# Kernel tuning notes

Hardware: AMD Instinct MI355X
Metric: run time of the kernel (lower is better)

## Reference

```python
import jax, jax.numpy as jnp
import numpy as np

DIM = 2048
N_HEADS = 32
N_KV_HEADS = 8
HEAD_DIM = DIM // N_HEADS  # 64
N_REP = N_HEADS // N_KV_HEADS  # 4
ROPE_BASE = 10000.0


def _rope_cos_sin(seq_len, head_dim, dtype):
    inv_freq = 1.0 / (ROPE_BASE ** (jnp.arange(0, head_dim, 2, dtype=jnp.float32) / head_dim))
    freqs = jnp.arange(seq_len, dtype=jnp.float32)[:, None] * inv_freq[None, :]  # [S, hd/2]
    return jnp.cos(freqs).astype(dtype), jnp.sin(freqs).astype(dtype)


def _apply_rope(x, cos, sin):
    # x: [B, S, H, hd]; cos/sin: [S, hd/2]
    x1, x2 = jnp.split(x, 2, axis=-1)
    c = cos[None, :, None, :]
    s = sin[None, :, None, :]
    return jnp.concatenate([x1 * c - x2 * s, x1 * s + x2 * c], axis=-1)


def setup_inputs() -> dict:
    key = jax.random.key(0)
    ks = jax.random.split(key, 5)
    B, S = 2, 2048
    x = jax.random.normal(ks[0], (B, S, DIM), dtype=jnp.float32)
    scale = 1.0 / np.sqrt(DIM)
    wq = jax.random.normal(ks[1], (DIM, DIM), dtype=jnp.float32) * scale
    wk = jax.random.normal(ks[2], (N_KV_HEADS * HEAD_DIM, DIM), dtype=jnp.float32) * scale
    wv = jax.random.normal(ks[3], (N_KV_HEADS * HEAD_DIM, DIM), dtype=jnp.float32) * scale
    wo = jax.random.normal(ks[4], (DIM, DIM), dtype=jnp.float32) * scale
    return {"x": x, "wq": wq, "wk": wk, "wv": wv, "wo": wo}


def reference(x, wq, wk, wv, wo):
    B, S, D = x.shape
    # projections (nn.Linear: y = x @ W.T)
    xq = (x @ wq.T).reshape(B, S, N_HEADS, HEAD_DIM)
    xk = (x @ wk.T).reshape(B, S, N_KV_HEADS, HEAD_DIM)
    xv = (x @ wv.T).reshape(B, S, N_KV_HEADS, HEAD_DIM)

    cos, sin = _rope_cos_sin(S, HEAD_DIM, x.dtype)
    xq = _apply_rope(xq, cos, sin)
    xk = _apply_rope(xk, cos, sin)

    # GQA: repeat kv heads
    keys = jnp.repeat(xk, N_REP, axis=2)    # [B, S, H, hd]
    values = jnp.repeat(xv, N_REP, axis=2)

    scores = jnp.einsum('bqhd,bkhd->bhqk', xq, keys) / np.sqrt(HEAD_DIM)
    causal = jnp.tril(jnp.ones((S, S), dtype=bool))
    scores = jnp.where(causal[None, None, :, :], scores, jnp.finfo(scores.dtype).min)
    probs = jax.nn.softmax(scores, axis=-1)
    out = jnp.einsum('bhqk,bkhd->bqhd', probs, values).reshape(B, S, D)
    return out @ wo.T  # dropout in eval mode == identity
```

## Files before the change

kernel.cpp:

```cpp
#include <hip/hip_runtime.h>

typedef __attribute__((ext_vector_type(8))) short bf16x8;
typedef __attribute__((ext_vector_type(4))) float f32x4;
typedef __attribute__((ext_vector_type(4))) unsigned short u16x4;

#define GPTR(p) (const __attribute__((address_space(1))) void*)(p)
#define LPTR(p) (__attribute__((address_space(3))) void*)(p)

static __device__ __forceinline__ unsigned short f2bf(float f) {
  union { float f; unsigned int u; } x; x.f = f;
  unsigned int u = x.u;
  unsigned int r = (u + 0x7fffu + ((u >> 16) & 1u)) >> 16;
  return (unsigned short)r;
}
static __device__ __forceinline__ float bf2f(unsigned short h) {
  union { unsigned int u; float f; } x; x.u = ((unsigned int)h) << 16;
  return x.f;
}
static __device__ __forceinline__ f32x4 f32x4_zero() {
  f32x4 z = {0.f, 0.f, 0.f, 0.f}; return z;
}
static __device__ __forceinline__ unsigned int cvt_pk_bf16(float lo, float hi) {
  unsigned int r;
  asm("v_cvt_pk_bf16_f32 %0, %1, %2" : "=v"(r) : "v"(lo), "v"(hi));
  return r;
}

__global__ void rope_table_kernel(float* __restrict__ costab, float* __restrict__ sintab) {
  int i = blockIdx.x * blockDim.x + threadIdx.x;
  int s = i >> 5, d = i & 31;
  float invf = exp2f(-(float)d * (13.287712379549449f / 32.0f));
  float a = (float)s * invf;
  costab[i] = cosf(a);
  sintab[i] = sinf(a);
}

__global__ void f32_to_bf16(const float* __restrict__ src, unsigned short* __restrict__ dst, int n4) {
  int stride = gridDim.x * blockDim.x;
  for (int i = blockIdx.x * blockDim.x + threadIdx.x; i < n4; i += stride) {
    float4 v = ((const float4*)src)[i];
    u16x4 o;
    o.x = f2bf(v.x); o.y = f2bf(v.y); o.z = f2bf(v.z); o.w = f2bf(v.w);
    *(u16x4*)(dst + (size_t)i * 4) = o;
  }
}

template<int OUT_BF16>
__global__ __launch_bounds__(256) void gemm_bt(const unsigned short* __restrict__ A,
                                               const unsigned short* __restrict__ B,
                                               void* __restrict__ Cv, int N, int K) {
  __shared__ __align__(16) unsigned short lsA[128 * 32];
  __shared__ __align__(16) unsigned short lsB[128 * 32];
  const int tid = threadIdx.x;
  const int wave = tid >> 6, lane = tid & 63;
  const int fq = lane >> 4, fr = lane & 15;
  const int wr = wave >> 1, wc = wave & 1;
  const int m0 = blockIdx.y * 128, n0 = blockIdx.x * 128;

  const unsigned short* ga0 = A + (size_t)(m0 + (tid >> 2)) * K + ((tid & 3) << 3);
  const unsigned short* ga1 = ga0 + (size_t)64 * K;
  const unsigned short* gb0 = B + (size_t)(n0 + (tid >> 2)) * K + ((tid & 3) << 3);
  const unsigned short* gb1 = gb0 + (size_t)64 * K;
  unsigned short* lA0 = lsA + wave * 512;
  unsigned short* lA1 = lsA + 2048 + wave * 512;
  unsigned short* lB0 = lsB + wave * 512;
  unsigned short* lB1 = lsB + 2048 + wave * 512;

  f32x4 acc[4][4];
#pragma unroll
  for (int i = 0; i < 4; ++i)
#pragma unroll
    for (int j = 0; j < 4; ++j) acc[i][j] = f32x4_zero();

  for (int k0 = 0; k0 < K; k0 += 32) {
    __syncthreads();
    __builtin_amdgcn_global_load_lds(GPTR(ga0 + k0), LPTR(lA0), 16, 0, 0);
    __builtin_amdgcn_global_load_lds(GPTR(ga1 + k0), LPTR(lA1), 16, 0, 0);
    __builtin_amdgcn_global_load_lds(GPTR(gb0 + k0), LPTR(lB0), 16, 0, 0);
    __builtin_amdgcn_global_load_lds(GPTR(gb1 + k0), LPTR(lB1), 16, 0, 0);
    __syncthreads();
    bf16x8 af[4], bfr[4];
#pragma unroll
    for (int f = 0; f < 4; ++f) {
      af[f]  = *(const bf16x8*)(lsA + (wr * 64 + f * 16 + fr) * 32 + fq * 8);
      bfr[f] = *(const bf16x8*)(lsB + (wc * 64 + f * 16 + fr) * 32 + fq * 8);
    }
#pragma unroll
    for (int i = 0; i < 4; ++i)
#pragma unroll
      for (int j = 0; j < 4; ++j)
        acc[i][j] = __builtin_amdgcn_mfma_f32_16x16x32_bf16(af[i], bfr[j], acc[i][j], 0, 0, 0);
  }

#pragma unroll
  for (int i = 0; i < 4; ++i) {
    const int row = m0 + wr * 64 + i * 16 + fq * 4;
#pragma unroll
    for (int j = 0; j < 4; ++j) {
      const int col = n0 + wc * 64 + j * 16 + fr;
#pragma unroll
      for (int v = 0; v < 4; ++v) {
        if (OUT_BF16) ((unsigned short*)Cv)[(size_t)(row + v) * N + col] = f2bf(acc[i][j][v]);
        else          ((float*)Cv)[(size_t)(row + v) * N + col] = acc[i][j][v];
      }
    }
  }
}

__global__ void rope_kernel(unsigned short* __restrict__ qkv,
                            const float* __restrict__ costab,
                            const float* __restrict__ sintab) {
  int idx = blockIdx.x * blockDim.x + threadIdx.x;
  if (idx >= 4096 * 1280) return;
  int row = idx / 1280;
  int p = idx - row * 1280;
  int s = row & 2047;
  int col, d; bool isq;
  if (p < 1024) { isq = true;  d = p & 31; col = (p >> 5) * 64 + d; }
  else { isq = false; int pk = p - 1024; d = pk & 31; col = 2048 + (pk >> 5) * 64 + d; }
  float c = costab[s * 32 + d], sn = sintab[s * 32 + d];
  unsigned short* base = qkv + (size_t)row * 3072;
  float x1 = bf2f(base[col]), x2 = bf2f(base[col + 32]);
  float o1 = x1 * c - x2 * sn;
  float o2 = x1 * sn + x2 * c;
  if (isq) { o1 *= 0.18033688011112042f; o2 *= 0.18033688011112042f; }
  base[col] = f2bf(o1);
  base[col + 32] = f2bf(o2);
}

#define KBLK 64
__global__ __launch_bounds__(256) void flash_attn(const unsigned short* __restrict__ qkv,
                                                  unsigned short* __restrict__ out) {
  __shared__ __align__(16) unsigned short K_lds[64 * 64];
  __shared__ __align__(16) unsigned short Vt_lds[64 * 64];
  __shared__ __align__(16) unsigned int  P_lds[4][32 * 36];

  const int tid = threadIdx.x;
  const int wave = tid >> 6, lane = tid & 63;
  const int fq = lane >> 4, fr = lane & 15;
  const int b = blockIdx.z, h = blockIdx.y;
  const int qt = gridDim.x - 1 - blockIdx.x;
  const int kvh = h >> 2;
  const int q0 = qt * 128;
  const int wq0 = q0 + wave * 32;

  bf16x8 qreg[2][2];
#pragma unroll
  for (int qf = 0; qf < 2; ++qf)
#pragma unroll
    for (int kk = 0; kk < 2; ++kk)
      qreg[qf][kk] = *(const bf16x8*)(qkv + (size_t)(b * 2048 + wq0 + qf * 16 + fr) * 3072
                                      + h * 64 + kk * 32 + fq * 8);

  f32x4 o_acc[4][2];
  float m_run[2], l_run[2];
#pragma unroll
  for (int dc = 0; dc < 4; ++dc) { o_acc[dc][0] = f32x4_zero(); o_acc[dc][1] = f32x4_zero(); }
  m_run[0] = m_run[1] = -1e30f;
  l_run[0] = l_run[1] = 0.f;

  const char* kgbase = (const char*)qkv + (size_t)(b * 2048) * 6144 + 4096 + kvh * 128;
  const unsigned short* vgbase = qkv + (size_t)(b * 2048) * 3072 + 2560 + kvh * 64;
  const int nsteps = (q0 + 128) >> 6;

  for (int st = 0; st < nsteps; ++st) {
    const int k0 = st << 6;
    __syncthreads();
#pragma unroll
    for (int r = 0; r < 2; ++r) {
      const int row = (tid >> 3) + r * 32;
      const int cb = (tid & 7) << 4;
      __builtin_amdgcn_global_load_lds(GPTR(kgbase + (size_t)(k0 + row) * 6144 + (cb ^ ((row & 7) << 4))),
                                       LPTR((char*)K_lds + r * 4096 + wave * 1024), 16, 0, 0);
    }
#pragma unroll
    for (int r = 0; r < 2; ++r) {
      const int k = (tid >> 3) + r * 32;
      const int c0 = (tid & 7) << 3;
      bf16x8 vv = *(const bf16x8*)(vgbase + (size_t)(k0 + k) * 3072 + c0);
#pragma unroll
      for (int j = 0; j < 8; ++j) {
        const int d = c0 + j;
        Vt_lds[d * 64 + (k & 7) + ((((k >> 3) ^ (d >> 3)) & 7) << 3)] = (unsigned short)vv[j];
      }
    }
    __syncthreads();

    if (k0 <= wq0 + 31) {
      f32x4 s[2][4];
#pragma unroll
      for (int qf = 0; qf < 2; ++qf)
#pragma unroll
        for (int kf = 0; kf < 4; ++kf) s[qf][kf] = f32x4_zero();
#pragma unroll
      for (int kf = 0; kf < 4; ++kf) {
        const int krow = kf * 16 + fr;
        const char* kb = (const char*)K_lds + krow * 128;
        const int swz = (krow & 7) << 4;
        bf16x8 kf0 = *(const bf16x8*)(kb + ((fq * 16) ^ swz));
        bf16x8 kf1 = *(const bf16x8*)(kb + ((64 + fq * 16) ^ swz));
#pragma unroll
        for (int qf = 0; qf < 2; ++qf) {
          s[qf][kf] = __builtin_amdgcn_mfma_f32_16x16x32_bf16(kf0, qreg[qf][0], s[qf][kf], 0, 0, 0);
          s[qf][kf] = __builtin_amdgcn_mfma_f32_16x16x32_bf16(kf1, qreg[qf][1], s[qf][kf], 0, 0, 0);
        }
      }
      if (k0 + 63 > wq0) {
#pragma unroll
        for (int qf = 0; qf < 2; ++qf) {
          const int q = wq0 + qf * 16 + fr;
#pragma unroll
          for (int kf = 0; kf < 4; ++kf)
#pragma unroll
            for (int v = 0; v < 4; ++v) {
              const int key = k0 + kf * 16 + fq * 4 + v;
              if (key > q) s[qf][kf][v] = -1e30f;
            }
        }
      }
#pragma unroll
      for (int qf = 0; qf < 2; ++qf) {
        float t = s[qf][0][0];
#pragma unroll
        for (int kf = 0; kf < 4; ++kf)
#pragma unroll
          for (int v = 0; v < 4; ++v) t = fmaxf(t, s[qf][kf][v]);
        t = fmaxf(t, __shfl_xor(t, 16));
        t = fmaxf(t, __shfl_xor(t, 32));
        const float mo = m_run[qf];
        const float mn = fmaxf(mo, t);
        const float sc = __builtin_amdgcn_exp2f(mo - mn);
        m_run[qf] = mn;
        float ps = 0.f;
#pragma unroll
        for (int kf = 0; kf < 4; ++kf)
#pragma unroll
          for (int v = 0; v < 4; ++v) {
            const float p = __builtin_amdgcn_exp2f(s[qf][kf][v] - mn);
            s[qf][kf][v] = p;
            ps += p;
          }
        ps += __shfl_xor(ps, 16);
        ps += __shfl_xor(ps, 32);
        l_run[qf] = l_run[qf] * sc + ps;
#pragma unroll
        for (int dc = 0; dc < 4; ++dc) o_acc[dc][qf] *= sc;
        unsigned int* pbase = &P_lds[wave][(qf * 16 + fr) * 36];
#pragma unroll
        for (int kf = 0; kf < 4; ++kf) {
          uint2 w;
          w.x = cvt_pk_bf16(s[qf][kf][0], s[qf][kf][1]);
          w.y = cvt_pk_bf16(s[qf][kf][2], s[qf][kf][3]);
          *(uint2*)(pbase + kf * 8 + fq * 2) = w;
        }
      }
#pragma unroll
      for (int kk = 0; kk < 2; ++kk) {
        bf16x8 pa0 = *(const bf16x8*)((const char*)&P_lds[wave][0] + (fr) * 144 + kk * 64 + fq * 16);
        bf16x8 pa1 = *(const bf16x8*)((const char*)&P_lds[wave][0] + (16 + fr) * 144 + kk * 64 + fq * 16);
#pragma unroll
        for (int dc = 0; dc < 4; ++dc) {
          const int d = dc * 16 + fr;
          bf16x8 vt = *(const bf16x8*)(Vt_lds + d * 64 + ((((kk * 4 + fq) ^ (d >> 3)) & 7) << 3));
          o_acc[dc][0] = __builtin_amdgcn_mfma_f32_16x16x32_bf16(vt, pa0, o_acc[dc][0], 0, 0, 0);
          o_acc[dc][1] = __builtin_amdgcn_mfma_f32_16x16x32_bf16(vt, pa1, o_acc[dc][1], 0, 0, 0);
        }
      }
    }
  }

#pragma unroll
  for (int qf = 0; qf < 2; ++qf) {
    const float inv = 1.0f / l_run[qf];
    const size_t row = (size_t)(b * 2048 + wq0 + qf * 16 + fr);
#pragma unroll
    for (int dc = 0; dc < 4; ++dc) {
      u16x4 o;
#pragma unroll
      for (int v = 0; v < 4; ++v) o[v] = f2bf(o_acc[dc][qf][v] * inv);
      *(u16x4*)(out + row * 2048 + h * 64 + dc * 16 + fq * 4) = o;
    }
  }
}

extern "C" void kernel_launch(void* const* d_in, const int* in_sizes, int n_in,
                              void* d_out, int out_size, void* d_ws, size_t ws_size,
                              hipStream_t stream) {
  (void)in_sizes; (void)n_in; (void)out_size; (void)ws_size;
  const float* x  = (const float*)d_in[0];
  const float* wq = (const float*)d_in[1];
  const float* wk = (const float*)d_in[2];
  const float* wv = (const float*)d_in[3];
  const float* wo = (const float*)d_in[4];

  char* wsb = (char*)d_ws;
  unsigned short* xb     = (unsigned short*)(wsb);
  unsigned short* attn_o = xb;
  unsigned short* wqkvb  = (unsigned short*)(wsb + 16777216);
  unsigned short* wob    = (unsigned short*)(wsb + 29360128);
  unsigned short* qkv    = (unsigned short*)(wsb + 37748736);
  float* costab          = (float*)(wsb + 62914560);
  float* sintab          = (float*)(wsb + 63176704);

  rope_table_kernel<<<256, 256, 0, stream>>>(costab, sintab);

  f32_to_bf16<<<2048, 256, 0, stream>>>(x,  xb,                 8388608 / 4);
  f32_to_bf16<<<1024, 256, 0, stream>>>(wq, wqkvb,              4194304 / 4);
  f32_to_bf16<<<256,  256, 0, stream>>>(wk, wqkvb + 4194304,    1048576 / 4);
  f32_to_bf16<<<256,  256, 0, stream>>>(wv, wqkvb + 5242880,    1048576 / 4);
  f32_to_bf16<<<1024, 256, 0, stream>>>(wo, wob,                4194304 / 4);

  gemm_bt<1><<<dim3(24, 32), 256, 0, stream>>>(xb, wqkvb, (void*)qkv, 3072, 2048);

  rope_kernel<<<20480, 256, 0, stream>>>(qkv, costab, sintab);

  flash_attn<<<dim3(16, 32, 2), 256, 0, stream>>>(qkv, attn_o);

  gemm_bt<0><<<dim3(16, 32), 256, 0, stream>>>(attn_o, wob, d_out, 2048, 2048);
}
```

Measured before the change: 310.1 us.

## Double-buffer K/V tiles in flash attention with 512-thread blocks and warp-specialized loads

```diff
diff --git a/kernel.cpp b/kernel.cpp
--- a/kernel.cpp
+++ b/kernel.cpp
@@ -128,12 +128,11 @@
   base[col + 32] = f2bf(o2);
 }
 
-#define KBLK 64
-__global__ __launch_bounds__(256) void flash_attn(const unsigned short* __restrict__ qkv,
-                                                  unsigned short* __restrict__ out) {
-  __shared__ __align__(16) unsigned short K_lds[64 * 64];
-  __shared__ __align__(16) unsigned short Vt_lds[64 * 64];
-  __shared__ __align__(16) unsigned int  P_lds[4][32 * 36];
+__global__ __launch_bounds__(512, 4) void flash_attn(const unsigned short* __restrict__ qkv,
+                                                     unsigned short* __restrict__ out) {
+  __shared__ __align__(16) char K_sh[2 * 8192];
+  __shared__ __align__(16) char V_sh[2 * 8192];
+  __shared__ __align__(16) char P_sh[8 * 4096];
 
   const int tid = threadIdx.x;
   const int wave = tid >> 6, lane = tid & 63;
@@ -141,8 +140,9 @@
   const int b = blockIdx.z, h = blockIdx.y;
   const int qt = gridDim.x - 1 - blockIdx.x;
   const int kvh = h >> 2;
-  const int q0 = qt * 128;
+  const int q0 = qt * 256;
   const int wq0 = q0 + wave * 32;
+  char* Pw = P_sh + wave * 4096;
 
   bf16x8 qreg[2][2];
 #pragma unroll
@@ -161,32 +161,61 @@
 
   const char* kgbase = (const char*)qkv + (size_t)(b * 2048) * 6144 + 4096 + kvh * 128;
   const unsigned short* vgbase = qkv + (size_t)(b * 2048) * 3072 + 2560 + kvh * 64;
-  const int nsteps = (q0 + 128) >> 6;
-
+  const int nsteps = (q0 + 256) >> 6;
+
+  const int vk2 = (tid >> 3) << 1;
+  const int vc0 = (tid & 7) << 3;
+  const int kt = tid - 256;
+
+  {
+    if (wave < 4) {
+      bf16x8 vv0 = *(const bf16x8*)(vgbase + (size_t)vk2 * 3072 + vc0);
+      bf16x8 vv1 = *(const bf16x8*)(vgbase + (size_t)(vk2 + 1) * 3072 + vc0);
+#pragma unroll
+      for (int j = 0; j < 8; ++j) {
+        const int d = vc0 + j;
+        const int G = ((d & 7) ^ (d >> 3)) & 7;
+        unsigned int w = ((unsigned int)(unsigned short)vv0[j]) |
+                         (((unsigned int)(unsigned short)vv1[j]) << 16);
+        *(unsigned int*)(V_sh + (d << 7) + ((vk2 << 1) ^ (G << 4))) = w;
+      }
+    } else {
+#pragma unroll
+      for (int ld = 0; ld < 2; ++ld) {
+        const int row = (kt >> 3) + (ld << 5);
+        const int cb = ((kt & 7) << 4) ^ ((row & 7) << 4);
+        __builtin_amdgcn_global_load_lds(GPTR(kgbase + (size_t)row * 6144 + cb),
+                                         LPTR(K_sh + kt * 16 + ld * 4096), 16, 0, 0);
+      }
+    }
+  }
+  __syncthreads();
+
+  int buf = 0;
   for (int st = 0; st < nsteps; ++st) {
     const int k0 = st << 6;
-    __syncthreads();
-#pragma unroll
-    for (int r = 0; r < 2; ++r) {
-      const int row = (tid >> 3) + r * 32;
-      const int cb = (tid & 7) << 4;
-      __builtin_amdgcn_global_load_lds(GPTR(kgbase + (size_t)(k0 + row) * 6144 + (cb ^ ((row & 7) << 4))),
-                                       LPTR((char*)K_lds + r * 4096 + wave * 1024), 16, 0, 0);
-    }
-#pragma unroll
-    for (int r = 0; r < 2; ++r) {
-      const int k = (tid >> 3) + r * 32;
-      const int c0 = (tid & 7) << 3;
-      bf16x8 vv = *(const bf16x8*)(vgbase + (size_t)(k0 + k) * 3072 + c0);
-#pragma unroll
-      for (int j = 0; j < 8; ++j) {
-        const int d = c0 + j;
-        Vt_lds[d * 64 + (k & 7) + ((((k >> 3) ^ (d >> 3)) & 7) << 3)] = (unsigned short)vv[j];
-      }
-    }
-    __syncthreads();
+    const bool has_next = (st + 1) < nsteps;
+    bf16x8 vv0, vv1;
+    if (has_next) {
+      const int k0n = k0 + 64;
+      if (wave < 4) {
+        vv0 = *(const bf16x8*)(vgbase + (size_t)(k0n + vk2) * 3072 + vc0);
+        vv1 = *(const bf16x8*)(vgbase + (size_t)(k0n + vk2 + 1) * 3072 + vc0);
+      } else {
+        char* Kn = K_sh + (buf ^ 1) * 8192;
+#pragma unroll
+        for (int ld = 0; ld < 2; ++ld) {
+          const int row = (kt >> 3) + (ld << 5);
+          const int cb = ((kt & 7) << 4) ^ ((row & 7) << 4);
+          __builtin_amdgcn_global_load_lds(GPTR(kgbase + (size_t)(k0n + row) * 6144 + cb),
+                                           LPTR(Kn + kt * 16 + ld * 4096), 16, 0, 0);
+        }
+      }
+    }
 
     if (k0 <= wq0 + 31) {
+      const char* Kb = K_sh + buf * 8192;
+      const char* Vb = V_sh + buf * 8192;
       f32x4 s[2][4];
 #pragma unroll
       for (int qf = 0; qf < 2; ++qf)
@@ -195,14 +224,13 @@
 #pragma unroll
       for (int kf = 0; kf < 4; ++kf) {
         const int krow = kf * 16 + fr;
-        const char* kb = (const char*)K_lds + krow * 128;
         const int swz = (krow & 7) << 4;
-        bf16x8 kf0 = *(const bf16x8*)(kb + ((fq * 16) ^ swz));
-        bf16x8 kf1 = *(const bf16x8*)(kb + ((64 + fq * 16) ^ swz));
+        bf16x8 ka = *(const bf16x8*)(Kb + krow * 128 + ((fq * 16) ^ swz));
+        bf16x8 kb = *(const bf16x8*)(Kb + krow * 128 + ((64 + fq * 16) ^ swz));
 #pragma unroll
         for (int qf = 0; qf < 2; ++qf) {
-          s[qf][kf] = __builtin_amdgcn_mfma_f32_16x16x32_bf16(kf0, qreg[qf][0], s[qf][kf], 0, 0, 0);
-          s[qf][kf] = __builtin_amdgcn_mfma_f32_16x16x32_bf16(kf1, qreg[qf][1], s[qf][kf], 0, 0, 0);
+          s[qf][kf] = __builtin_amdgcn_mfma_f32_16x16x32_bf16(ka, qreg[qf][0], s[qf][kf], 0, 0, 0);
+          s[qf][kf] = __builtin_amdgcn_mfma_f32_16x16x32_bf16(kb, qreg[qf][1], s[qf][kf], 0, 0, 0);
         }
       }
       if (k0 + 63 > wq0) {
@@ -245,28 +273,47 @@
         l_run[qf] = l_run[qf] * sc + ps;
 #pragma unroll
         for (int dc = 0; dc < 4; ++dc) o_acc[dc][qf] *= sc;
-        unsigned int* pbase = &P_lds[wave][(qf * 16 + fr) * 36];
+        const int r = qf * 16 + fr;
+        const int rswz = (r & 7) << 4;
 #pragma unroll
         for (int kf = 0; kf < 4; ++kf) {
           uint2 w;
           w.x = cvt_pk_bf16(s[qf][kf][0], s[qf][kf][1]);
           w.y = cvt_pk_bf16(s[qf][kf][2], s[qf][kf][3]);
-          *(uint2*)(pbase + kf * 8 + fq * 2) = w;
-        }
-      }
+          *(uint2*)(Pw + r * 128 + ((kf * 32 + fq * 8) ^ rswz)) = w;
+        }
+      }
+      asm volatile("s_waitcnt lgkmcnt(0)" ::: "memory");
+      __builtin_amdgcn_sched_barrier(0);
+      const int fswz = (fr & 7) << 4;
 #pragma unroll
       for (int kk = 0; kk < 2; ++kk) {
-        bf16x8 pa0 = *(const bf16x8*)((const char*)&P_lds[wave][0] + (fr) * 144 + kk * 64 + fq * 16);
-        bf16x8 pa1 = *(const bf16x8*)((const char*)&P_lds[wave][0] + (16 + fr) * 144 + kk * 64 + fq * 16);
+        bf16x8 pa0 = *(const bf16x8*)(Pw + fr * 128 + ((kk * 64 + fq * 16) ^ fswz));
+        bf16x8 pa1 = *(const bf16x8*)(Pw + (16 + fr) * 128 + ((kk * 64 + fq * 16) ^ fswz));
 #pragma unroll
         for (int dc = 0; dc < 4; ++dc) {
           const int d = dc * 16 + fr;
-          bf16x8 vt = *(const bf16x8*)(Vt_lds + d * 64 + ((((kk * 4 + fq) ^ (d >> 3)) & 7) << 3));
+          const int G = ((d & 7) ^ (d >> 3)) & 7;
+          bf16x8 vt = *(const bf16x8*)(Vb + d * 128 + ((kk * 64 + fq * 16) ^ (G << 4)));
           o_acc[dc][0] = __builtin_amdgcn_mfma_f32_16x16x32_bf16(vt, pa0, o_acc[dc][0], 0, 0, 0);
           o_acc[dc][1] = __builtin_amdgcn_mfma_f32_16x16x32_bf16(vt, pa1, o_acc[dc][1], 0, 0, 0);
         }
       }
     }
+
+    if (has_next && wave < 4) {
+      char* Vn = V_sh + (buf ^ 1) * 8192;
+#pragma unroll
+      for (int j = 0; j < 8; ++j) {
+        const int d = vc0 + j;
+        const int G = ((d & 7) ^ (d >> 3)) & 7;
+        unsigned int w = ((unsigned int)(unsigned short)vv0[j]) |
+                         (((unsigned int)(unsigned short)vv1[j]) << 16);
+        *(unsigned int*)(Vn + (d << 7) + ((vk2 << 1) ^ (G << 4))) = w;
+      }
+    }
+    __syncthreads();
+    buf ^= 1;
   }
 
 #pragma unroll
@@ -314,7 +361,7 @@
 
   rope_kernel<<<20480, 256, 0, stream>>>(qkv, costab, sintab);
 
-  flash_attn<<<dim3(16, 32, 2), 256, 0, stream>>>(qkv, attn_o);
+  flash_attn<<<dim3(8, 32, 2), 512, 0, stream>>>(qkv, attn_o);
 
   gemm_bt<0><<<dim3(16, 32), 256, 0, stream>>>(attn_o, wob, d_out, 2048, 2048);
 }
```

After: 276.8 us. 1.12x faster.
